# Kernel optimization log

Measured on AMD Instinct MI355X. Metric: run time of the kernel, lower is better.

The kernel has to match this reference:

```python
import jax, jax.numpy as jnp
import numpy as np

K = 2  # DyReLU-B number of linear pieces
LAMBDAS = np.array([1.0, 1.0, 0.5, 0.5], dtype=np.float32)
INIT_V = np.array([1.0, 0.0, 0.0, 0.0], dtype=np.float32)
H_RATIO, W_RATIO = 0.05, 0.1


def _se(x, w1, w2):
    # Standard SE: global avg pool -> fc -> relu -> fc -> sigmoid -> channel scale
    y = x.mean(axis=(2, 3))                      # (b,c)
    y = jax.nn.relu(y @ w1.T)                    # (b,c//16)
    y = jax.nn.sigmoid(y @ w2.T)                 # (b,c)
    return x * y[:, :, None, None]


def _dyrelu(v, fc1w, fc1b, fc2w, fc2b):
    # DyReLU-B on pooled (b,c) vector (spatial dims of input are 1x1 here)
    b, c = v.shape
    theta = jax.nn.relu(v @ fc1w.T + fc1b)
    theta = theta @ fc2w.T + fc2b                # (b, 2K*c)
    theta = 2.0 * jax.nn.sigmoid(theta) - 1.0
    coefs = theta.reshape(b, c, 2 * K) * jnp.asarray(LAMBDAS) + jnp.asarray(INIT_V)
    a, bb = coefs[..., :K], coefs[..., K:]       # each (b,c,K)
    return jnp.max(v[..., None] * a + bb, axis=-1)  # (b,c)


def reference(x, se_w1, se_w2, ch_w, ch_b, cw_w, cw_b,
              dh_fc1w, dh_fc1b, dh_fc2w, dh_fc2b,
              dw_fc1w, dw_fc1b, dw_fc2w, dw_fc2b):
    b, c, h, w = x.shape
    x = _se(x, se_w1, se_w2)
    g = x.mean(axis=(2, 3))                      # adaptive_avg_pool2d -> (b,c)
    # 1x1 conv on (b,c,1,1) == linear on (b,c)
    sx = jax.nn.sigmoid(_dyrelu(g @ ch_w.T + ch_b, dh_fc1w, dh_fc1b, dh_fc2w, dh_fc2b))
    sy = jax.nn.sigmoid(_dyrelu(g @ cw_w.T + cw_b, dw_fc1w, dw_fc1b, dw_fc2w, dw_fc2b))
    sx = jnp.ceil(h * sx)
    sy = jnp.ceil(h * sy)                        # NOTE: original code scales sy by h, not w
    rh = int(H_RATIO * h)
    rw = int(W_RATIO * w)
    sx = jnp.minimum(sx, float(h - rh))[:, :, None, None]   # (b,c,1,1)
    sy = jnp.minimum(sy, float(w - rw))[:, :, None, None]
    rows = jnp.arange(h, dtype=x.dtype)[None, None, :, None]
    cols = jnp.arange(w, dtype=x.dtype)[None, None, None, :]
    # Vectorized replacement of the per-(sample,channel) rectangular zeroing loop
    inside = (rows >= sx) & (rows < sx + rh) & (cols >= sy) & (cols < sy + rw)
    return x * (~inside).astype(x.dtype)


def setup_inputs() -> dict:
    key = jax.random.key(0)
    ks = jax.random.split(key, 16)
    b, c, h, w = 32, 256, 64, 64
    r_se, r_dy = 16, 4
    s = 0.05
    return {
        "x": jax.random.normal(ks[0], (b, c, h, w), jnp.float32),
        "se_w1": jax.random.normal(ks[1], (c // r_se, c), jnp.float32) * s,
        "se_w2": jax.random.normal(ks[2], (c, c // r_se), jnp.float32) * s,
        "ch_w": jax.random.normal(ks[3], (c, c), jnp.float32) * s,
        "ch_b": jax.random.normal(ks[4], (c,), jnp.float32) * s,
        "cw_w": jax.random.normal(ks[5], (c, c), jnp.float32) * s,
        "cw_b": jax.random.normal(ks[6], (c,), jnp.float32) * s,
        "dh_fc1w": jax.random.normal(ks[7], (c // r_dy, c), jnp.float32) * s,
        "dh_fc1b": jax.random.normal(ks[8], (c // r_dy,), jnp.float32) * s,
        "dh_fc2w": jax.random.normal(ks[9], (2 * K * c, c // r_dy), jnp.float32) * s,
        "dh_fc2b": jax.random.normal(ks[10], (2 * K * c,), jnp.float32) * s,
        "dw_fc1w": jax.random.normal(ks[11], (c // r_dy, c), jnp.float32) * s,
        "dw_fc1b": jax.random.normal(ks[12], (c // r_dy,), jnp.float32) * s,
        "dw_fc2w": jax.random.normal(ks[13], (2 * K * c, c // r_dy), jnp.float32) * s,
        "dw_fc2b": jax.random.normal(ks[14], (2 * K * c,), jnp.float32) * s,
    }
```

## Files before the change

kernel.cpp:

```cpp
#include <hip/hip_runtime.h>
#include <math.h>


#define BATCH 32
#define CH 256
#define HW 64
#define PLANE (HW * HW)
#define NPLANES (BATCH * CH)

__device__ __forceinline__ float sigf(float x) { return 1.0f / (1.0f + expf(-x)); }

__global__ __launch_bounds__(256) void transpose_weights(
    const float* __restrict__ ch_w, const float* __restrict__ cw_w,
    const float* __restrict__ dh1,  const float* __restrict__ dw1,
    const float* __restrict__ dh2,  const float* __restrict__ dw2,
    float* __restrict__ chT, float* __restrict__ cwT,
    float* __restrict__ dh1T, float* __restrict__ dw1T,
    float* __restrict__ dh2T, float* __restrict__ dw2T)
{
    int idx = blockIdx.x * 256 + threadIdx.x;
    if (idx < 65536) {
        int r = idx >> 8, c = idx & 255;
        chT[c * 256 + r] = ch_w[idx];
    } else if (idx < 131072) {
        int i = idx - 65536; int r = i >> 8, c = i & 255;
        cwT[c * 256 + r] = cw_w[i];
    } else if (idx < 147456) {
        int i = idx - 131072; int r = i >> 8, c = i & 255;
        dh1T[c * 64 + r] = dh1[i];
    } else if (idx < 163840) {
        int i = idx - 147456; int r = i >> 8, c = i & 255;
        dw1T[c * 64 + r] = dw1[i];
    } else if (idx < 229376) {
        int i = idx - 163840; int r = i >> 6, c = i & 63;
        dh2T[c * 1024 + r] = dh2[i];
    } else if (idx < 294912) {
        int i = idx - 229376; int r = i >> 6, c = i & 63;
        dw2T[c * 1024 + r] = dw2[i];
    }
}

__global__ __launch_bounds__(256) void mean_kernel(const float* __restrict__ x,
                                                   float* __restrict__ mean)
{
    int wid = threadIdx.x >> 6, lane = threadIdx.x & 63;
    int p = blockIdx.x * 4 + wid;
    const float4* xp = (const float4*)(x + (size_t)p * PLANE);
    float s = 0.f;
#pragma unroll
    for (int k = 0; k < 16; ++k) {
        float4 v = xp[lane + 64 * k];
        s += (v.x + v.y) + (v.z + v.w);
    }
#pragma unroll
    for (int off = 32; off; off >>= 1) s += __shfl_xor(s, off, 64);
    if (lane == 0) mean[p] = s * (1.f / 4096.f);
}

__global__ __launch_bounds__(256) void mlp_kernel(
    const float* __restrict__ mean,
    const float* __restrict__ se_w1, const float* __restrict__ se_w2,
    const float* __restrict__ ch_b,  const float* __restrict__ cw_b,
    const float* __restrict__ dh1b,  const float* __restrict__ dh2b,
    const float* __restrict__ dw1b,  const float* __restrict__ dw2b,
    const float* __restrict__ chT,   const float* __restrict__ cwT,
    const float* __restrict__ dh1T,  const float* __restrict__ dw1T,
    const float* __restrict__ dh2T,  const float* __restrict__ dw2T,
    float* __restrict__ scale, int* __restrict__ sx, int* __restrict__ sy)
{
    __shared__ float m_sh[256], t1_sh[16], g_sh[256], vh_sh[256], vw_sh[256];
    __shared__ float th1h_sh[64], th1w_sh[64], th2h_sh[1024], th2w_sh[1024];

    int b = blockIdx.x, t = threadIdx.x;
    m_sh[t] = mean[b * 256 + t];
    __syncthreads();

    if (t < 16) {
        float s = 0.f;
        for (int c = 0; c < 256; ++c) s = fmaf(m_sh[c], se_w1[t * 256 + c], s);
        t1_sh[t] = fmaxf(s, 0.f);
    }
    __syncthreads();

    float acc = 0.f;
#pragma unroll
    for (int j = 0; j < 16; ++j) acc = fmaf(t1_sh[j], se_w2[t * 16 + j], acc);
    float y = sigf(acc);
    float g = m_sh[t] * y;
    g_sh[t] = g;
    scale[b * 256 + t] = y;
    __syncthreads();

    float vh = ch_b[t], vw = cw_b[t];
#pragma unroll 4
    for (int j = 0; j < 256; ++j) {
        float gj = g_sh[j];
        vh = fmaf(gj, chT[j * 256 + t], vh);
        vw = fmaf(gj, cwT[j * 256 + t], vw);
    }
    vh_sh[t] = vh; vw_sh[t] = vw;
    __syncthreads();

    if (t < 64) {
        float s = dh1b[t];
#pragma unroll 4
        for (int c = 0; c < 256; ++c) s = fmaf(vh_sh[c], dh1T[c * 64 + t], s);
        th1h_sh[t] = fmaxf(s, 0.f);
    } else if (t < 128) {
        int r = t - 64;
        float s = dw1b[r];
#pragma unroll 4
        for (int c = 0; c < 256; ++c) s = fmaf(vw_sh[c], dw1T[c * 64 + r], s);
        th1w_sh[r] = fmaxf(s, 0.f);
    }
    __syncthreads();

    float ah0 = 0, ah1 = 0, ah2 = 0, ah3 = 0;
    float aw0 = 0, aw1 = 0, aw2 = 0, aw3 = 0;
#pragma unroll 4
    for (int j = 0; j < 64; ++j) {
        float sh = th1h_sh[j], sw = th1w_sh[j];
        const float* ph = dh2T + j * 1024 + t;
        const float* pw = dw2T + j * 1024 + t;
        ah0 = fmaf(sh, ph[0], ah0);   ah1 = fmaf(sh, ph[256], ah1);
        ah2 = fmaf(sh, ph[512], ah2); ah3 = fmaf(sh, ph[768], ah3);
        aw0 = fmaf(sw, pw[0], aw0);   aw1 = fmaf(sw, pw[256], aw1);
        aw2 = fmaf(sw, pw[512], aw2); aw3 = fmaf(sw, pw[768], aw3);
    }
    th2h_sh[t      ] = ah0 + dh2b[t      ];
    th2h_sh[t + 256] = ah1 + dh2b[t + 256];
    th2h_sh[t + 512] = ah2 + dh2b[t + 512];
    th2h_sh[t + 768] = ah3 + dh2b[t + 768];
    th2w_sh[t      ] = aw0 + dw2b[t      ];
    th2w_sh[t + 256] = aw1 + dw2b[t + 256];
    th2w_sh[t + 512] = aw2 + dw2b[t + 512];
    th2w_sh[t + 768] = aw3 + dw2b[t + 768];
    __syncthreads();

    const float LAM[4] = {1.f, 1.f, 0.5f, 0.5f};
    const float INI[4] = {1.f, 0.f, 0.f, 0.f};
    float coh[4], cow[4];
#pragma unroll
    for (int i = 0; i < 4; ++i) {
        float thh = 2.f * sigf(th2h_sh[t * 4 + i]) - 1.f;
        float thw = 2.f * sigf(th2w_sh[t * 4 + i]) - 1.f;
        coh[i] = thh * LAM[i] + INI[i];
        cow[i] = thw * LAM[i] + INI[i];
    }
    float uh = fmaxf(vh * coh[0] + coh[2], vh * coh[1] + coh[3]);
    float uw = fmaxf(vw * cow[0] + cow[2], vw * cow[1] + cow[3]);
    float sxf = fminf(ceilf(64.f * sigf(uh)), 61.f);
    float syf = fminf(ceilf(64.f * sigf(uw)), 58.f);
    sx[b * 256 + t] = (int)sxf;
    sy[b * 256 + t] = (int)syf;
}

__global__ __launch_bounds__(256) void apply_kernel(
    const float* __restrict__ x, const float* __restrict__ scale,
    const int* __restrict__ sx, const int* __restrict__ sy,
    float* __restrict__ out)
{
    int p = blockIdx.x;
    float s = scale[p];
    int rx = sx[p], cy = sy[p];
    const float4* xp = (const float4*)(x + (size_t)p * PLANE);
    float4* op = (float4*)(out + (size_t)p * PLANE);
    int t = threadIdx.x;
#pragma unroll
    for (int q = 0; q < 4; ++q) {
        int i4 = t + 256 * q;
        float4 v = xp[i4];
        int row = i4 >> 4;
        int col0 = (i4 & 15) * 4;
        bool rin = (row >= rx) && (row < rx + 3);
        float4 o;
        o.x = (rin && col0     >= cy && col0     < cy + 6) ? 0.f : v.x * s;
        o.y = (rin && col0 + 1 >= cy && col0 + 1 < cy + 6) ? 0.f : v.y * s;
        o.z = (rin && col0 + 2 >= cy && col0 + 2 < cy + 6) ? 0.f : v.z * s;
        o.w = (rin && col0 + 3 >= cy && col0 + 3 < cy + 6) ? 0.f : v.w * s;
        op[i4] = o;
    }
}

extern "C" void kernel_launch(void* const* d_in, const int* in_sizes, int n_in,
                              void* d_out, int out_size, void* d_ws, size_t ws_size,
                              hipStream_t stream)
{
    const float* x      = (const float*)d_in[0];
    const float* se_w1  = (const float*)d_in[1];
    const float* se_w2  = (const float*)d_in[2];
    const float* ch_w   = (const float*)d_in[3];
    const float* ch_b   = (const float*)d_in[4];
    const float* cw_w   = (const float*)d_in[5];
    const float* cw_b   = (const float*)d_in[6];
    const float* dh1w   = (const float*)d_in[7];
    const float* dh1b   = (const float*)d_in[8];
    const float* dh2w   = (const float*)d_in[9];
    const float* dh2b   = (const float*)d_in[10];
    const float* dw1w   = (const float*)d_in[11];
    const float* dw1b   = (const float*)d_in[12];
    const float* dw2w   = (const float*)d_in[13];
    const float* dw2b   = (const float*)d_in[14];
    float* out = (float*)d_out;

    float* ws    = (float*)d_ws;
    float* meanb = ws;
    float* scale = ws + 8192;
    int*   sxp   = (int*)(ws + 16384);
    int*   syp   = (int*)(ws + 24576);
    float* chT   = ws + 32768;
    float* cwT   = chT + 65536;
    float* dh1T  = cwT + 65536;
    float* dw1T  = dh1T + 16384;
    float* dh2T  = dw1T + 16384;
    float* dw2T  = dh2T + 65536;

    transpose_weights<<<1152, 256, 0, stream>>>(ch_w, cw_w, dh1w, dw1w, dh2w, dw2w,
                                                chT, cwT, dh1T, dw1T, dh2T, dw2T);
    mean_kernel<<<NPLANES / 4, 256, 0, stream>>>(x, meanb);
    mlp_kernel<<<BATCH, 256, 0, stream>>>(meanb, se_w1, se_w2, ch_b, cw_b,
                                          dh1b, dh2b, dw1b, dw2b,
                                          chT, cwT, dh1T, dw1T, dh2T, dw2T,
                                          scale, sxp, syp);
    apply_kernel<<<NPLANES, 256, 0, stream>>>(x, scale, sxp, syp, out);
}
```

Measured before the change: 327.2 us.

## Split MLP kernel across branches and parallelize its serial reductions

```diff
diff --git a/kernel.cpp b/kernel.cpp
--- a/kernel.cpp
+++ b/kernel.cpp
@@ -7,6 +7,8 @@
 #define HW 64
 #define PLANE (HW * HW)
 #define NPLANES (BATCH * CH)
+
+typedef float vf4 __attribute__((ext_vector_type(4)));
 
 __device__ __forceinline__ float sigf(float x) { return 1.0f / (1.0f + expf(-x)); }
 
@@ -45,13 +47,16 @@
 {
     int wid = threadIdx.x >> 6, lane = threadIdx.x & 63;
     int p = blockIdx.x * 4 + wid;
-    const float4* xp = (const float4*)(x + (size_t)p * PLANE);
-    float s = 0.f;
-#pragma unroll
-    for (int k = 0; k < 16; ++k) {
-        float4 v = xp[lane + 64 * k];
-        s += (v.x + v.y) + (v.z + v.w);
-    }
+    const vf4* xp = (const vf4*)(x + (size_t)p * PLANE);
+    float s0 = 0.f, s1 = 0.f;
+#pragma unroll
+    for (int k = 0; k < 16; k += 2) {
+        vf4 v0 = xp[lane + 64 * k];
+        vf4 v1 = xp[lane + 64 * (k + 1)];
+        s0 += (v0.x + v0.y) + (v0.z + v0.w);
+        s1 += (v1.x + v1.y) + (v1.z + v1.w);
+    }
+    float s = s0 + s1;
 #pragma unroll
     for (int off = 32; off; off >>= 1) s += __shfl_xor(s, off, 64);
     if (lane == 0) mean[p] = s * (1.f / 4096.f);
@@ -61,98 +66,104 @@
     const float* __restrict__ mean,
     const float* __restrict__ se_w1, const float* __restrict__ se_w2,
     const float* __restrict__ ch_b,  const float* __restrict__ cw_b,
-    const float* __restrict__ dh1b,  const float* __restrict__ dh2b,
-    const float* __restrict__ dw1b,  const float* __restrict__ dw2b,
+    const float* __restrict__ dh1b,  const float* __restrict__ dw1b,
+    const float* __restrict__ dh2b,  const float* __restrict__ dw2b,
     const float* __restrict__ chT,   const float* __restrict__ cwT,
     const float* __restrict__ dh1T,  const float* __restrict__ dw1T,
     const float* __restrict__ dh2T,  const float* __restrict__ dw2T,
     float* __restrict__ scale, int* __restrict__ sx, int* __restrict__ sy)
 {
-    __shared__ float m_sh[256], t1_sh[16], g_sh[256], vh_sh[256], vw_sh[256];
-    __shared__ float th1h_sh[64], th1w_sh[64], th2h_sh[1024], th2w_sh[1024];
-
-    int b = blockIdx.x, t = threadIdx.x;
+    __shared__ float m_sh[256], part_sh[16][17], t1_sh[16];
+    __shared__ float g_sh[256], v_sh[256], red_sh[4][64];
+    __shared__ float th1_sh[64], th2_sh[1024];
+
+    int b = blockIdx.x >> 1, br = blockIdx.x & 1;
+    const float* cT  = br ? cwT  : chT;
+    const float* cb  = br ? cw_b : ch_b;
+    const float* f1T = br ? dw1T : dh1T;
+    const float* f1b = br ? dw1b : dh1b;
+    const float* f2T = br ? dw2T : dh2T;
+    const float* f2b = br ? dw2b : dh2b;
+    int*  so  = br ? sy : sx;
+    float lim = br ? 58.f : 61.f;
+
+    int t = threadIdx.x;
     m_sh[t] = mean[b * 256 + t];
     __syncthreads();
 
+    {
+        int o = t & 15, part = t >> 4;
+        const float* w = se_w1 + o * 256 + part * 16;
+        const float* mm = m_sh + part * 16;
+        float s = 0.f;
+#pragma unroll
+        for (int j = 0; j < 16; ++j) s = fmaf(mm[j], w[j], s);
+        part_sh[o][part] = s;
+    }
+    __syncthreads();
     if (t < 16) {
+        float a = 0.f;
+#pragma unroll
+        for (int p = 0; p < 16; ++p) a += part_sh[t][p];
+        t1_sh[t] = fmaxf(a, 0.f);
+    }
+    __syncthreads();
+
+    {
+        float acc = 0.f;
+#pragma unroll
+        for (int j = 0; j < 16; ++j) acc = fmaf(t1_sh[j], se_w2[t * 16 + j], acc);
+        float y = sigf(acc);
+        g_sh[t] = m_sh[t] * y;
+        if (br == 0) scale[b * 256 + t] = y;
+    }
+    __syncthreads();
+
+    float v = cb[t];
+#pragma unroll 8
+    for (int j = 0; j < 256; ++j) v = fmaf(g_sh[j], cT[j * 256 + t], v);
+    v_sh[t] = v;
+    __syncthreads();
+
+    {
+        int o = t & 63, part = t >> 6;
+        const float* vs = v_sh + part * 64;
         float s = 0.f;
-        for (int c = 0; c < 256; ++c) s = fmaf(m_sh[c], se_w1[t * 256 + c], s);
-        t1_sh[t] = fmaxf(s, 0.f);
-    }
-    __syncthreads();
-
-    float acc = 0.f;
-#pragma unroll
-    for (int j = 0; j < 16; ++j) acc = fmaf(t1_sh[j], se_w2[t * 16 + j], acc);
-    float y = sigf(acc);
-    float g = m_sh[t] * y;
-    g_sh[t] = g;
-    scale[b * 256 + t] = y;
-    __syncthreads();
-
-    float vh = ch_b[t], vw = cw_b[t];
-#pragma unroll 4
-    for (int j = 0; j < 256; ++j) {
-        float gj = g_sh[j];
-        vh = fmaf(gj, chT[j * 256 + t], vh);
-        vw = fmaf(gj, cwT[j * 256 + t], vw);
-    }
-    vh_sh[t] = vh; vw_sh[t] = vw;
-    __syncthreads();
-
-    if (t < 64) {
-        float s = dh1b[t];
-#pragma unroll 4
-        for (int c = 0; c < 256; ++c) s = fmaf(vh_sh[c], dh1T[c * 64 + t], s);
-        th1h_sh[t] = fmaxf(s, 0.f);
-    } else if (t < 128) {
-        int r = t - 64;
-        float s = dw1b[r];
-#pragma unroll 4
-        for (int c = 0; c < 256; ++c) s = fmaf(vw_sh[c], dw1T[c * 64 + r], s);
-        th1w_sh[r] = fmaxf(s, 0.f);
-    }
-    __syncthreads();
-
-    float ah0 = 0, ah1 = 0, ah2 = 0, ah3 = 0;
-    float aw0 = 0, aw1 = 0, aw2 = 0, aw3 = 0;
-#pragma unroll 4
+#pragma unroll 8
+        for (int j = 0; j < 64; ++j) s = fmaf(vs[j], f1T[(part * 64 + j) * 64 + o], s);
+        red_sh[part][o] = s;
+    }
+    __syncthreads();
+    if (t < 64)
+        th1_sh[t] = fmaxf(red_sh[0][t] + red_sh[1][t] + red_sh[2][t] + red_sh[3][t] + f1b[t], 0.f);
+    __syncthreads();
+
+    float a0 = 0, a1 = 0, a2 = 0, a3 = 0;
+#pragma unroll 8
     for (int j = 0; j < 64; ++j) {
-        float sh = th1h_sh[j], sw = th1w_sh[j];
-        const float* ph = dh2T + j * 1024 + t;
-        const float* pw = dw2T + j * 1024 + t;
-        ah0 = fmaf(sh, ph[0], ah0);   ah1 = fmaf(sh, ph[256], ah1);
-        ah2 = fmaf(sh, ph[512], ah2); ah3 = fmaf(sh, ph[768], ah3);
-        aw0 = fmaf(sw, pw[0], aw0);   aw1 = fmaf(sw, pw[256], aw1);
-        aw2 = fmaf(sw, pw[512], aw2); aw3 = fmaf(sw, pw[768], aw3);
-    }
-    th2h_sh[t      ] = ah0 + dh2b[t      ];
-    th2h_sh[t + 256] = ah1 + dh2b[t + 256];
-    th2h_sh[t + 512] = ah2 + dh2b[t + 512];
-    th2h_sh[t + 768] = ah3 + dh2b[t + 768];
-    th2w_sh[t      ] = aw0 + dw2b[t      ];
-    th2w_sh[t + 256] = aw1 + dw2b[t + 256];
-    th2w_sh[t + 512] = aw2 + dw2b[t + 512];
-    th2w_sh[t + 768] = aw3 + dw2b[t + 768];
+        float s1 = th1_sh[j];
+        const float* p = f2T + j * 1024 + t;
+        a0 = fmaf(s1, p[0],   a0);
+        a1 = fmaf(s1, p[256], a1);
+        a2 = fmaf(s1, p[512], a2);
+        a3 = fmaf(s1, p[768], a3);
+    }
+    th2_sh[t      ] = a0 + f2b[t      ];
+    th2_sh[t + 256] = a1 + f2b[t + 256];
+    th2_sh[t + 512] = a2 + f2b[t + 512];
+    th2_sh[t + 768] = a3 + f2b[t + 768];
     __syncthreads();
 
     const float LAM[4] = {1.f, 1.f, 0.5f, 0.5f};
     const float INI[4] = {1.f, 0.f, 0.f, 0.f};
-    float coh[4], cow[4];
+    float co[4];
 #pragma unroll
     for (int i = 0; i < 4; ++i) {
-        float thh = 2.f * sigf(th2h_sh[t * 4 + i]) - 1.f;
-        float thw = 2.f * sigf(th2w_sh[t * 4 + i]) - 1.f;
-        coh[i] = thh * LAM[i] + INI[i];
-        cow[i] = thw * LAM[i] + INI[i];
-    }
-    float uh = fmaxf(vh * coh[0] + coh[2], vh * coh[1] + coh[3]);
-    float uw = fmaxf(vw * cow[0] + cow[2], vw * cow[1] + cow[3]);
-    float sxf = fminf(ceilf(64.f * sigf(uh)), 61.f);
-    float syf = fminf(ceilf(64.f * sigf(uw)), 58.f);
-    sx[b * 256 + t] = (int)sxf;
-    sy[b * 256 + t] = (int)syf;
+        float th = 2.f * sigf(th2_sh[t * 4 + i]) - 1.f;
+        co[i] = th * LAM[i] + INI[i];
+    }
+    float u = fmaxf(v * co[0] + co[2], v * co[1] + co[3]);
+    so[b * 256 + t] = (int)fminf(ceilf(64.f * sigf(u)), lim);
 }
 
 __global__ __launch_bounds__(256) void apply_kernel(
@@ -163,17 +174,17 @@
     int p = blockIdx.x;
     float s = scale[p];
     int rx = sx[p], cy = sy[p];
-    const float4* xp = (const float4*)(x + (size_t)p * PLANE);
-    float4* op = (float4*)(out + (size_t)p * PLANE);
+    const vf4* xp = (const vf4*)(x + (size_t)p * PLANE);
+    vf4* op = (vf4*)(out + (size_t)p * PLANE);
     int t = threadIdx.x;
 #pragma unroll
     for (int q = 0; q < 4; ++q) {
         int i4 = t + 256 * q;
-        float4 v = xp[i4];
+        vf4 v = xp[i4];
         int row = i4 >> 4;
         int col0 = (i4 & 15) * 4;
         bool rin = (row >= rx) && (row < rx + 3);
-        float4 o;
+        vf4 o;
         o.x = (rin && col0     >= cy && col0     < cy + 6) ? 0.f : v.x * s;
         o.y = (rin && col0 + 1 >= cy && col0 + 1 < cy + 6) ? 0.f : v.y * s;
         o.z = (rin && col0 + 2 >= cy && col0 + 2 < cy + 6) ? 0.f : v.z * s;
@@ -218,9 +229,9 @@
     transpose_weights<<<1152, 256, 0, stream>>>(ch_w, cw_w, dh1w, dw1w, dh2w, dw2w,
                                                 chT, cwT, dh1T, dw1T, dh2T, dw2T);
     mean_kernel<<<NPLANES / 4, 256, 0, stream>>>(x, meanb);
-    mlp_kernel<<<BATCH, 256, 0, stream>>>(meanb, se_w1, se_w2, ch_b, cw_b,
-                                          dh1b, dh2b, dw1b, dw2b,
-                                          chT, cwT, dh1T, dw1T, dh2T, dw2T,
-                                          scale, sxp, syp);
+    mlp_kernel<<<BATCH * 2, 256, 0, stream>>>(meanb, se_w1, se_w2, ch_b, cw_b,
+                                              dh1b, dw1b, dh2b, dw2b,
+                                              chT, cwT, dh1T, dw1T, dh2T, dw2T,
+                                              scale, sxp, syp);
     apply_kernel<<<NPLANES, 256, 0, stream>>>(x, scale, sxp, syp, out);
 }
```

Result: faster. 298.5 us (-8.8%).
